# Optimization experiments

Hardware: AMD Instinct MI355X
Metric: run time of the kernel (lower is better)

## Reference

```python
import jax, jax.numpy as jnp
import numpy as np

N = 100000      # nodes
E = 3200000     # edges (avg degree 32, undirected)
FIN = 256
FOUT = 256
K = 4


def setup_inputs() -> dict:
    key = jax.random.key(0)
    k1, k2, k3 = jax.random.split(key, 3)
    x = jax.random.normal(k1, (N, FIN), dtype=jnp.float32)
    edge_index = jax.random.randint(k2, (2, E), 0, N, dtype=jnp.int32)
    stdv = 1.0 / np.sqrt(FIN * K)
    # K per-hop dense projection weights, uniform(-stdv, stdv) as in reset_parameters
    weights = jax.random.uniform(k3, (K, FIN, FOUT), dtype=jnp.float32,
                                 minval=-stdv, maxval=stdv)
    return {"x": x, "edge_index": edge_index, "weights": weights}


def reference(x, edge_index, weights):
    # edge_index -> symmetric adjacency S (from_edgelist builds an undirected graph):
    # spmm(S, z)[i] = sum over neighbors j of z[j]; scatter-add both directions.
    src, dst = edge_index[0], edge_index[1]

    def spmm(z):
        out = jnp.zeros_like(z).at[dst].add(z[src])
        return out.at[src].add(z[dst])

    zs = [x]
    for _ in range(1, weights.shape[0]):
        x = spmm(x)           # [N, Fin] k-hop diffused features
        zs.append(x)
    # sum_k zs[k] @ weights[k]  -> [N, Fout]
    return jnp.einsum('knf,kfo->no', jnp.stack(zs), weights)
```

## Files before the change

kernel.cpp:

```cpp
#include <hip/hip_runtime.h>
#include <hip/hip_bf16.h>


#define NNODES 100000
#define NEDGES 3200000
#define FOUTF  256
#define MPAD   100096
#define MTILES 782
#define NB     782
#define FILLB  1024
#define CHUNK  3125

typedef __attribute__((ext_vector_type(4))) int   i32x4;
typedef __attribute__((ext_vector_type(4))) float f32x4;

__device__ __forceinline__ void async_ld16(const void* g, void* l) {
  __builtin_amdgcn_global_load_lds(
      (const __attribute__((address_space(1))) unsigned int*)g,
      (__attribute__((address_space(3))) unsigned int*)l, 16, 0, 0);
}


__global__ __launch_bounds__(256)
void bucket_count_kernel(const int* __restrict__ ei, int* __restrict__ bcount) {
  __shared__ int h[NB];
  for (int i = threadIdx.x; i < NB; i += 256) h[i] = 0;
  __syncthreads();
  for (int e = blockIdx.x * 256 + threadIdx.x; e < NEDGES; e += gridDim.x * 256) {
    int s = ei[e];
    int d = ei[NEDGES + e];
    atomicAdd(&h[d >> 7], 1);
    atomicAdd(&h[s >> 7], 1);
  }
  __syncthreads();
  for (int i = threadIdx.x; i < NB; i += 256) {
    int c = h[i];
    if (c) atomicAdd(&bcount[i], c);
  }
}

__global__ __launch_bounds__(1024)
void bucket_scan_kernel(const int* __restrict__ bcount, int* __restrict__ bbase,
                        int* __restrict__ bcursor) {
  __shared__ int ws[16];
  int t = threadIdx.x, lane = t & 63, wv = t >> 6;
  int v = (t < NB) ? bcount[t] : 0;
  int s = v;
  #pragma unroll
  for (int off = 1; off < 64; off <<= 1) {
    int tmp = __shfl_up(s, off, 64);
    if (lane >= off) s += tmp;
  }
  if (lane == 63) ws[wv] = s;
  __syncthreads();
  if (t == 0) {
    int run = 0;
    #pragma unroll
    for (int k = 0; k < 16; ++k) { int tmp = ws[k]; ws[k] = run; run += tmp; }
  }
  __syncthreads();
  int excl = s + ws[wv] - v;
  if (t < NB) { bbase[t] = excl; bcursor[t] = excl; }
  if (t == NB) bbase[NB] = excl;
}

__global__ __launch_bounds__(256)
void bin_fill_kernel(const int* __restrict__ ei, int* __restrict__ bcursor,
                     unsigned int* __restrict__ binned) {
  __shared__ int h[NB];
  for (int i = threadIdx.x; i < NB; i += 256) h[i] = 0;
  __syncthreads();
  const int e0 = blockIdx.x * CHUNK;
  const int e1 = (e0 + CHUNK < NEDGES) ? e0 + CHUNK : NEDGES;
  for (int e = e0 + threadIdx.x; e < e1; e += 256) {
    int s = ei[e];
    int d = ei[NEDGES + e];
    atomicAdd(&h[d >> 7], 1);
    atomicAdd(&h[s >> 7], 1);
  }
  __syncthreads();
  for (int i = threadIdx.x; i < NB; i += 256) {
    int c = h[i];
    h[i] = c ? atomicAdd(&bcursor[i], c) : 0;
  }
  __syncthreads();
  for (int e = e0 + threadIdx.x; e < e1; e += 256) {
    int s = ei[e];
    int d = ei[NEDGES + e];
    int p = atomicAdd(&h[d >> 7], 1);
    binned[p] = ((unsigned int)(d & 127) << 17) | (unsigned int)s;
    int q = atomicAdd(&h[s >> 7], 1);
    binned[q] = ((unsigned int)(s & 127) << 17) | (unsigned int)d;
  }
}

__global__ __launch_bounds__(256)
void bucket_csr_kernel(const unsigned int* __restrict__ binned,
                       const int* __restrict__ bbase,
                       int* __restrict__ row_ptr, int* __restrict__ adj) {
  __shared__ int cnt[128];
  __shared__ int cur[128];
  const int b = blockIdx.x;
  const int node0 = b << 7;
  const int base = bbase[b];
  const int end = bbase[b + 1];
  const int tid = threadIdx.x;
  if (tid < 128) cnt[tid] = 0;
  __syncthreads();
  for (int i = base + tid; i < end; i += 256) {
    unsigned int v = binned[i];
    atomicAdd(&cnt[v >> 17], 1);
  }
  __syncthreads();
  if (tid < 128) {
    int ex = 0;
    #pragma unroll 8
    for (int j = 0; j < 128; ++j) {
      int c = cnt[j];
      ex += (j < tid) ? c : 0;
    }
    int node = node0 + tid;
    if (node < NNODES) row_ptr[node] = base + ex;
    cur[tid] = base + ex;
  }
  if (tid == 0 && b == NB - 1) row_ptr[NNODES] = end;
  __syncthreads();
  for (int i = base + tid; i < end; i += 256) {
    unsigned int v = binned[i];
    int nbr = (int)(v & 0x1FFFFu);
    int p = atomicAdd(&cur[v >> 17], 1);
    adj[p] = nbr << 8;
  }
}


__global__ __launch_bounds__(256)
void convert_x_kernel(const float* __restrict__ x,
                      unsigned char* __restrict__ g0,
                      float* __restrict__ sc0) {
  const int row = (blockIdx.x * 256 + threadIdx.x) >> 6;
  const int lane = threadIdx.x & 63;
  if (row >= NNODES) return;
  float4 xv = *(const float4*)&x[(size_t)row * 256 + (lane << 2)];

  float m = fmaxf(fmaxf(fabsf(xv.x), fabsf(xv.y)), fmaxf(fabsf(xv.z), fabsf(xv.w)));
  #pragma unroll
  for (int i = 1; i < 64; i <<= 1) m = fmaxf(m, __shfl_xor(m, i, 64));
  float inv = (m > 0.f) ? 127.f / m : 0.f;
  int q0 = (int)__builtin_rintf(xv.x * inv);
  int q1 = (int)__builtin_rintf(xv.y * inv);
  int q2 = (int)__builtin_rintf(xv.z * inv);
  int q3 = (int)__builtin_rintf(xv.w * inv);
  *(unsigned int*)(g0 + (size_t)row * 256 + (lane << 2)) =
      ((unsigned)q0 & 255u) | (((unsigned)q1 & 255u) << 8) |
      (((unsigned)q2 & 255u) << 16) | (((unsigned)q3 & 255u) << 24);
  if (lane == 0) sc0[row] = m * (1.f / 127.f);
}

__global__ void wmax_kernel(const float* __restrict__ w, float* __restrict__ dW) {
  __shared__ float red[4];
  const int k = blockIdx.x;
  const float* wk = w + (size_t)k * 65536;
  float m = 0.f;
  for (int i = threadIdx.x; i < 65536; i += 256) m = fmaxf(m, fabsf(wk[i]));
  #pragma unroll
  for (int i = 1; i < 64; i <<= 1) m = fmaxf(m, __shfl_xor(m, i, 64));
  if ((threadIdx.x & 63) == 0) red[threadIdx.x >> 6] = m;
  __syncthreads();
  if (threadIdx.x == 0) {
    m = fmaxf(fmaxf(red[0], red[1]), fmaxf(red[2], red[3]));
    dW[k] = m * (1.f / 127.f);
    dW[4 + k] = (m > 0.f) ? 127.f / m : 0.f;
  }
}

__global__ void quantw_kernel(const float* __restrict__ w, const float* __restrict__ dW,
                              signed char* __restrict__ W8) {
  int idx = blockIdx.x * 256 + threadIdx.x;
  int k = idx >> 16, o = (idx >> 8) & 255, f = idx & 255;
  float inv = dW[4 + k];
  W8[idx] = (signed char)(int)__builtin_rintf(w[(size_t)(k * 256 + f) * 256 + o] * inv);
}


#define DECQ(vv, ss)                                        \
  { acc0 += (ss) * (float)((vv) & 255u);                    \
    acc1 += (ss) * (float)(((vv) >> 8) & 255u);             \
    acc2 += (ss) * (float)(((vv) >> 16) & 255u);            \
    acc3 += (ss) * (float)((vv) >> 24);                     \
    ssum += (ss); }

__global__ __launch_bounds__(256)
void spmm_q8_kernel(const unsigned char* __restrict__ gin,
                    const float* __restrict__ sin,
                    unsigned char* __restrict__ gout,
                    float* __restrict__ sout,
                    const int* __restrict__ row_ptr,
                    const int* __restrict__ adjb) {
  const int wid = __builtin_amdgcn_readfirstlane((blockIdx.x * 256 + threadIdx.x) >> 6);
  const int lane = threadIdx.x & 63;
  if (wid >= NNODES) return;
  const int beg = row_ptr[wid];
  const int end = row_ptr[wid + 1];
  const int lb = lane << 2;
  const char* scb = (const char*)sin;

  float acc0 = 0.f, acc1 = 0.f, acc2 = 0.f, acc3 = 0.f, ssum = 0.f;
  int j = beg;
  for (; j + 4 <= end; j += 4) {
    int o0 = adjb[j + 0], o1 = adjb[j + 1], o2 = adjb[j + 2], o3 = adjb[j + 3];
    float s0 = *(const float*)(scb + (o0 >> 6));
    float s1 = *(const float*)(scb + (o1 >> 6));
    float s2 = *(const float*)(scb + (o2 >> 6));
    float s3 = *(const float*)(scb + (o3 >> 6));
    unsigned int v0 = *(const unsigned int*)(gin + o0 + lb) ^ 0x80808080u;
    unsigned int v1 = *(const unsigned int*)(gin + o1 + lb) ^ 0x80808080u;
    unsigned int v2 = *(const unsigned int*)(gin + o2 + lb) ^ 0x80808080u;
    unsigned int v3 = *(const unsigned int*)(gin + o3 + lb) ^ 0x80808080u;
    DECQ(v0, s0); DECQ(v1, s1); DECQ(v2, s2); DECQ(v3, s3);
  }
  for (; j < end; ++j) {
    int o = adjb[j];
    float s = *(const float*)(scb + (o >> 6));
    unsigned int v = *(const unsigned int*)(gin + o + lb) ^ 0x80808080u;
    DECQ(v, s);
  }

  const float bias = 128.f * ssum;
  const float a0 = acc0 - bias;
  const float a1 = acc1 - bias;
  const float a2 = acc2 - bias;
  const float a3 = acc3 - bias;

  float m = fmaxf(fmaxf(fabsf(a0), fabsf(a1)), fmaxf(fabsf(a2), fabsf(a3)));
  #pragma unroll
  for (int i = 1; i < 64; i <<= 1) m = fmaxf(m, __shfl_xor(m, i, 64));
  float inv = (m > 0.f) ? 127.f / m : 0.f;
  int q0 = (int)__builtin_rintf(a0 * inv);
  int q1 = (int)__builtin_rintf(a1 * inv);
  int q2 = (int)__builtin_rintf(a2 * inv);
  int q3 = (int)__builtin_rintf(a3 * inv);
  *(unsigned int*)(gout + (size_t)wid * 256 + lb) =
      ((unsigned)q0 & 255u) | (((unsigned)q1 & 255u) << 8) |
      (((unsigned)q2 & 255u) << 16) | (((unsigned)q3 & 255u) << 24);
  if (lane == 0) sout[wid] = m * (1.f / 127.f);
}


__global__ __launch_bounds__(512)
void gemm_i8_kernel(const unsigned char* __restrict__ q0p,
                    const unsigned char* __restrict__ q1p,
                    const unsigned char* __restrict__ q2p,
                    const unsigned char* __restrict__ q3p,
                    const float* __restrict__ s0p,
                    const float* __restrict__ s1p,
                    const float* __restrict__ s2p,
                    const float* __restrict__ s3p,
                    const signed char* __restrict__ W8,
                    const float* __restrict__ dW,
                    float* __restrict__ C) {
  __shared__ __align__(16) unsigned char As[128 * 64];
  __shared__ __align__(16) unsigned char Bs[256 * 64];
  const int tid = threadIdx.x;
  const int lane = tid & 63;
  const int wave = tid >> 6;
  const int wr = wave >> 2;
  const int wc = wave & 3;
  const int rowA_base = blockIdx.x * 128;

  const unsigned char* qs[4] = {q0p, q1p, q2p, q3p};
  const float* scs[4] = {s0p, s1p, s2p, s3p};

  const int st_row = tid >> 2;
  const int st_kb = (tid & 3) << 4;

  f32x4 accf[4][4] = {};

  #pragma unroll
  for (int k = 0; k < 4; ++k) {
    const unsigned char* Qk = qs[k];
    const signed char* Wk = W8 + (size_t)k * 65536;
    i32x4 acci[4][4] = {};
    for (int k0 = 0; k0 < 256; k0 += 64) {
      __syncthreads();
      async_ld16(Qk + (size_t)(rowA_base + st_row) * 256 + k0 + st_kb,
                 &As[st_row * 64 + st_kb]);
      async_ld16(Wk + (size_t)st_row * 256 + k0 + st_kb,
                 &Bs[st_row * 64 + st_kb]);
      async_ld16(Wk + (size_t)(128 + st_row) * 256 + k0 + st_kb,
                 &Bs[(128 + st_row) * 64 + st_kb]);
      __syncthreads();
      i32x4 a[4], b[4];
      #pragma unroll
      for (int m = 0; m < 4; ++m)
        a[m] = *(const i32x4*)&As[(wr * 64 + m * 16 + (lane & 15)) * 64 + (lane >> 4) * 16];
      #pragma unroll
      for (int n = 0; n < 4; ++n)
        b[n] = *(const i32x4*)&Bs[(wc * 64 + n * 16 + (lane & 15)) * 64 + (lane >> 4) * 16];
      #pragma unroll
      for (int m = 0; m < 4; ++m) {
        #pragma unroll
        for (int n = 0; n < 4; ++n)
          acci[m][n] = __builtin_amdgcn_mfma_i32_16x16x64_i8(a[m], b[n], acci[m][n], 0, 0, 0);
      }
    }
    const float dWk = dW[k];
    const float* sk = scs[k];
    #pragma unroll
    for (int m = 0; m < 4; ++m) {
      #pragma unroll
      for (int j = 0; j < 4; ++j) {
        int r = rowA_base + wr * 64 + ((lane >> 4) << 2) + m * 16 + j;
        float s = sk[r] * dWk;
        #pragma unroll
        for (int n = 0; n < 4; ++n)
          accf[m][n][j] += s * (float)acci[m][n][j];
      }
    }
  }

  const int ccol0 = wc * 64 + (lane & 15);
  const int crow0 = rowA_base + wr * 64 + ((lane >> 4) << 2);
  #pragma unroll
  for (int m = 0; m < 4; ++m) {
    #pragma unroll
    for (int j = 0; j < 4; ++j) {
      int r = crow0 + m * 16 + j;
      if (r < NNODES) {
        float* cp = C + (size_t)r * FOUTF + ccol0;
        #pragma unroll
        for (int n = 0; n < 4; ++n) cp[n * 16] = accf[m][n][j];
      }
    }
  }
}


extern "C" void kernel_launch(void* const* d_in, const int* in_sizes, int n_in,
                              void* d_out, int out_size, void* d_ws, size_t ws_size,
                              hipStream_t stream) {
  (void)in_sizes; (void)n_in; (void)out_size; (void)ws_size;
  const float* x  = (const float*)d_in[0];
  const int*   ei = (const int*)d_in[1];
  const float* w  = (const float*)d_in[2];
  float* out = (float*)d_out;

  char* ws = (char*)d_ws;
  size_t off = 0;
  auto carve = [&](size_t bytes) -> void* {
    void* p = ws + off;
    off = (off + bytes + 255) & ~(size_t)255;
    return p;
  };
  unsigned char* gA = (unsigned char*)carve((size_t)MPAD * 256);
  unsigned char* gB = (unsigned char*)carve((size_t)MPAD * 256);
  unsigned char* gC = (unsigned char*)carve((size_t)MPAD * 256);
  unsigned char* gD = (unsigned char*)carve((size_t)MPAD * 256);
  float* scA        = (float*)carve((size_t)MPAD * 4);
  float* scB        = (float*)carve((size_t)MPAD * 4);
  float* scC        = (float*)carve((size_t)MPAD * 4);
  float* scD        = (float*)carve((size_t)MPAD * 4);
  signed char* W8   = (signed char*)carve((size_t)4 * 65536);
  float* dW         = (float*)carve(8 * 4);
  int* row_ptr      = (int*)carve((size_t)(NNODES + 1) * 4);
  int* adj          = (int*)carve((size_t)2 * NEDGES * 4);
  int* bcount       = (int*)carve((size_t)(NB + 1) * 4);
  int* bbase        = (int*)carve((size_t)(NB + 1) * 4);
  int* bcursor      = (int*)carve((size_t)(NB + 1) * 4);
  unsigned int* binned = (unsigned int*)gD;

  hipMemsetAsync(bcount, 0, (size_t)(NB + 1) * 4, stream);

  bucket_count_kernel<<<1024, 256, 0, stream>>>(ei, bcount);
  bucket_scan_kernel<<<1, 1024, 0, stream>>>(bcount, bbase, bcursor);
  bin_fill_kernel<<<FILLB, 256, 0, stream>>>(ei, bcursor, binned);
  bucket_csr_kernel<<<NB, 256, 0, stream>>>(binned, bbase, row_ptr, adj);

  convert_x_kernel<<<25000, 256, 0, stream>>>(x, gA, scA);
  wmax_kernel<<<4, 256, 0, stream>>>(w, dW);
  quantw_kernel<<<1024, 256, 0, stream>>>(w, dW, W8);

  spmm_q8_kernel<<<25000, 256, 0, stream>>>(gA, scA, gB, scB, row_ptr, adj);
  spmm_q8_kernel<<<25000, 256, 0, stream>>>(gB, scB, gC, scC, row_ptr, adj);
  spmm_q8_kernel<<<25000, 256, 0, stream>>>(gC, scC, gD, scD, row_ptr, adj);

  gemm_i8_kernel<<<MTILES, 512, 0, stream>>>(gA, gB, gC, gD, scA, scB, scC, scD,
                                             W8, dW, out);
}
```

Baseline: 1.087 ms.

## Parallelize weight max reduction and widen GEMM K-tile with XOR-swizzled LDS

The weight absmax reduction now spreads across 256 blocks with an atomicMax on float bits, where before it ran on only 4 serial blocks. The weight quantizer now reads coalesced and scatters its writes transposed. The int8 GEMM stages 128-wide K chunks, halving the barrier rounds, and XOR-swizzles the LDS layout to avoid bank conflicts on the MFMA operand reads. The cost is doubled LDS use per block, which may lower occupancy, plus an extra memset.

```diff
diff --git a/kernel.cpp b/kernel.cpp
--- a/kernel.cpp
+++ b/kernel.cpp
@@ -157,29 +157,33 @@
   if (lane == 0) sc0[row] = m * (1.f / 127.f);
 }
 
-__global__ void wmax_kernel(const float* __restrict__ w, float* __restrict__ dW) {
+__global__ __launch_bounds__(256)
+void wmax_kernel(const float* __restrict__ w, unsigned int* __restrict__ dWmax) {
   __shared__ float red[4];
-  const int k = blockIdx.x;
-  const float* wk = w + (size_t)k * 65536;
+  const int k = blockIdx.x >> 6;
+  const int chunk = blockIdx.x & 63;
+  const float* wk = w + (size_t)k * 65536 + chunk * 1024;
   float m = 0.f;
-  for (int i = threadIdx.x; i < 65536; i += 256) m = fmaxf(m, fabsf(wk[i]));
+  #pragma unroll
+  for (int i = 0; i < 4; ++i) m = fmaxf(m, fabsf(wk[threadIdx.x + i * 256]));
   #pragma unroll
   for (int i = 1; i < 64; i <<= 1) m = fmaxf(m, __shfl_xor(m, i, 64));
   if ((threadIdx.x & 63) == 0) red[threadIdx.x >> 6] = m;
   __syncthreads();
   if (threadIdx.x == 0) {
     m = fmaxf(fmaxf(red[0], red[1]), fmaxf(red[2], red[3]));
-    dW[k] = m * (1.f / 127.f);
-    dW[4 + k] = (m > 0.f) ? 127.f / m : 0.f;
-  }
-}
-
-__global__ void quantw_kernel(const float* __restrict__ w, const float* __restrict__ dW,
+    atomicMax(&dWmax[k], __float_as_uint(m));
+  }
+}
+
+__global__ void quantw_kernel(const float* __restrict__ w,
+                              const unsigned int* __restrict__ dWmax,
                               signed char* __restrict__ W8) {
   int idx = blockIdx.x * 256 + threadIdx.x;
-  int k = idx >> 16, o = (idx >> 8) & 255, f = idx & 255;
-  float inv = dW[4 + k];
-  W8[idx] = (signed char)(int)__builtin_rintf(w[(size_t)(k * 256 + f) * 256 + o] * inv);
+  int k = idx >> 16, f = (idx >> 8) & 255, o = idx & 255;
+  float mx = __uint_as_float(dWmax[k]);
+  float inv = (mx > 0.f) ? 127.f / mx : 0.f;
+  W8[(size_t)k * 65536 + o * 256 + f] = (signed char)(int)__builtin_rintf(w[idx] * inv);
 }
 
 
@@ -257,10 +261,10 @@
                     const float* __restrict__ s2p,
                     const float* __restrict__ s3p,
                     const signed char* __restrict__ W8,
-                    const float* __restrict__ dW,
+                    const unsigned int* __restrict__ dWmax,
                     float* __restrict__ C) {
-  __shared__ __align__(16) unsigned char As[128 * 64];
-  __shared__ __align__(16) unsigned char Bs[256 * 64];
+  __shared__ __align__(16) unsigned char As[128 * 128];
+  __shared__ __align__(16) unsigned char Bs[256 * 128];
   const int tid = threadIdx.x;
   const int lane = tid & 63;
   const int wave = tid >> 6;
@@ -271,9 +275,6 @@
   const unsigned char* qs[4] = {q0p, q1p, q2p, q3p};
   const float* scs[4] = {s0p, s1p, s2p, s3p};
 
-  const int st_row = tid >> 2;
-  const int st_kb = (tid & 3) << 4;
-
   f32x4 accf[4][4] = {};
 
   #pragma unroll
@@ -281,30 +282,48 @@
     const unsigned char* Qk = qs[k];
     const signed char* Wk = W8 + (size_t)k * 65536;
     i32x4 acci[4][4] = {};
-    for (int k0 = 0; k0 < 256; k0 += 64) {
+    #pragma unroll
+    for (int kc = 0; kc < 2; ++kc) {
       __syncthreads();
-      async_ld16(Qk + (size_t)(rowA_base + st_row) * 256 + k0 + st_kb,
-                 &As[st_row * 64 + st_kb]);
-      async_ld16(Wk + (size_t)st_row * 256 + k0 + st_kb,
-                 &Bs[st_row * 64 + st_kb]);
-      async_ld16(Wk + (size_t)(128 + st_row) * 256 + k0 + st_kb,
-                 &Bs[(128 + st_row) * 64 + st_kb]);
+      #pragma unroll
+      for (int i = 0; i < 2; ++i) {
+        int slot = tid + 512 * i;
+        int row = slot >> 3;
+        int col = ((slot & 7) << 4) ^ ((row & 7) << 4);
+        async_ld16(Qk + (size_t)(rowA_base + row) * 256 + kc * 128 + col,
+                   &As[slot * 16]);
+      }
+      #pragma unroll
+      for (int i = 0; i < 4; ++i) {
+        int slot = tid + 512 * i;
+        int row = slot >> 3;
+        int col = ((slot & 7) << 4) ^ ((row & 7) << 4);
+        async_ld16(Wk + (size_t)row * 256 + kc * 128 + col, &Bs[slot * 16]);
+      }
       __syncthreads();
-      i32x4 a[4], b[4];
       #pragma unroll
-      for (int m = 0; m < 4; ++m)
-        a[m] = *(const i32x4*)&As[(wr * 64 + m * 16 + (lane & 15)) * 64 + (lane >> 4) * 16];
-      #pragma unroll
-      for (int n = 0; n < 4; ++n)
-        b[n] = *(const i32x4*)&Bs[(wc * 64 + n * 16 + (lane & 15)) * 64 + (lane >> 4) * 16];
-      #pragma unroll
-      for (int m = 0; m < 4; ++m) {
+      for (int kk = 0; kk < 2; ++kk) {
+        const int kb = kk * 64 + ((lane >> 4) << 4);
+        i32x4 a[4], b[4];
         #pragma unroll
-        for (int n = 0; n < 4; ++n)
-          acci[m][n] = __builtin_amdgcn_mfma_i32_16x16x64_i8(a[m], b[n], acci[m][n], 0, 0, 0);
+        for (int m = 0; m < 4; ++m) {
+          int row = wr * 64 + m * 16 + (lane & 15);
+          a[m] = *(const i32x4*)&As[row * 128 + (kb ^ ((row & 7) << 4))];
+        }
+        #pragma unroll
+        for (int n = 0; n < 4; ++n) {
+          int row = wc * 64 + n * 16 + (lane & 15);
+          b[n] = *(const i32x4*)&Bs[row * 128 + (kb ^ ((row & 7) << 4))];
+        }
+        #pragma unroll
+        for (int m = 0; m < 4; ++m) {
+          #pragma unroll
+          for (int n = 0; n < 4; ++n)
+            acci[m][n] = __builtin_amdgcn_mfma_i32_16x16x64_i8(a[m], b[n], acci[m][n], 0, 0, 0);
+        }
       }
     }
-    const float dWk = dW[k];
+    const float dWk = __uint_as_float(dWmax[k]) * (1.f / 127.f);
     const float* sk = scs[k];
     #pragma unroll
     for (int m = 0; m < 4; ++m) {
@@ -361,7 +380,7 @@
   float* scC        = (float*)carve((size_t)MPAD * 4);
   float* scD        = (float*)carve((size_t)MPAD * 4);
   signed char* W8   = (signed char*)carve((size_t)4 * 65536);
-  float* dW         = (float*)carve(8 * 4);
+  unsigned int* dWmax = (unsigned int*)carve(4 * 4);
   int* row_ptr      = (int*)carve((size_t)(NNODES + 1) * 4);
   int* adj          = (int*)carve((size_t)2 * NEDGES * 4);
   int* bcount       = (int*)carve((size_t)(NB + 1) * 4);
@@ -370,6 +389,7 @@
   unsigned int* binned = (unsigned int*)gD;
 
   hipMemsetAsync(bcount, 0, (size_t)(NB + 1) * 4, stream);
+  hipMemsetAsync(dWmax, 0, 16, stream);
 
   bucket_count_kernel<<<1024, 256, 0, stream>>>(ei, bcount);
   bucket_scan_kernel<<<1, 1024, 0, stream>>>(bcount, bbase, bcursor);
@@ -377,13 +397,13 @@
   bucket_csr_kernel<<<NB, 256, 0, stream>>>(binned, bbase, row_ptr, adj);
 
   convert_x_kernel<<<25000, 256, 0, stream>>>(x, gA, scA);
-  wmax_kernel<<<4, 256, 0, stream>>>(w, dW);
-  quantw_kernel<<<1024, 256, 0, stream>>>(w, dW, W8);
+  wmax_kernel<<<256, 256, 0, stream>>>(w, dWmax);
+  quantw_kernel<<<1024, 256, 0, stream>>>(w, dWmax, W8);
 
   spmm_q8_kernel<<<25000, 256, 0, stream>>>(gA, scA, gB, scB, row_ptr, adj);
   spmm_q8_kernel<<<25000, 256, 0, stream>>>(gB, scB, gC, scC, row_ptr, adj);
   spmm_q8_kernel<<<25000, 256, 0, stream>>>(gC, scC, gD, scD, row_ptr, adj);
 
   gemm_i8_kernel<<<MTILES, 512, 0, stream>>>(gA, gB, gC, gD, scA, scB, scC, scD,
-                                             W8, dW, out);
-}
+                                             W8, dWmax, out);
+}
```

After: 1.028 ms. 5.4% less time.
